# Kernel tuning notes

Measured on AMD Instinct MI355X. Metric: run time of the kernel, lower is better.

Reference implementation:

```python
import jax, jax.numpy as jnp
import numpy as np

EMBED_DIM = 1024
NUM_HEADS = 16
D_K = EMBED_DIM // NUM_HEADS


def setup_inputs() -> dict:
    key = jax.random.key(0)
    kx, kq, kk, kv, ko = jax.random.split(key, 5)
    scale = 1.0 / np.sqrt(EMBED_DIM)
    return {
        "x": jax.random.normal(kx, (4, 2048, EMBED_DIM), dtype=jnp.float32),
        # nn.Linear weights are [out, in]; we store them the same way.
        "w_q": jax.random.normal(kq, (EMBED_DIM, EMBED_DIM), dtype=jnp.float32) * scale,
        "w_k": jax.random.normal(kk, (EMBED_DIM, EMBED_DIM), dtype=jnp.float32) * scale,
        "w_v": jax.random.normal(kv, (EMBED_DIM, EMBED_DIM), dtype=jnp.float32) * scale,
        "w_o": jax.random.normal(ko, (EMBED_DIM, EMBED_DIM), dtype=jnp.float32) * scale,
    }


def reference(x, w_q, w_k, w_v, w_o):
    B, S, E = x.shape
    H, Dk = NUM_HEADS, D_K

    def proj(w):  # [B,S,E] @ [E,E]^T -> [B,H,S,Dk]
        y = jnp.einsum('bse,fe->bsf', x, w)
        return y.reshape(B, S, H, Dk).transpose(0, 2, 1, 3)

    q, k, v = proj(w_q), proj(w_k), proj(w_v)
    scores = jnp.einsum('bhsd,bhtd->bhst', q, k) / jnp.sqrt(jnp.float32(Dk))
    attn = jax.nn.softmax(scores, axis=-1)  # dropout p=0 -> identity
    out = jnp.einsum('bhst,bhtd->bhsd', attn, v)
    out = out.transpose(0, 2, 1, 3).reshape(B, S, E)
    return jnp.einsum('bse,fe->bsf', out, w_o)
```

## Files before the change

### kernel.cpp

```cpp
#include <hip/hip_runtime.h>
#include <stdint.h>

typedef unsigned short u16;
typedef __attribute__((ext_vector_type(8))) short bf16x8;
typedef __attribute__((ext_vector_type(4))) float f32x4;
typedef __attribute__((ext_vector_type(16))) float f32x16;

#define EMB 1024
#define SLEN 2048
#define NHD 16
#define DKH 64

__device__ __forceinline__ u16 f2bf(float f) {
  uint32_t u = __float_as_uint(f);
  u = (u + 0x7fffu + ((u >> 16) & 1u)) >> 16;
  return (u16)u;
}

__device__ __forceinline__ void load_lds16(const void* g, void* l) {
  __builtin_amdgcn_global_load_lds(
      (const __attribute__((address_space(1))) uint32_t*)g,
      (__attribute__((address_space(3))) uint32_t*)l, 16, 0, 0);
}

__global__ __launch_bounds__(256) void cvt_all(
    const float* __restrict__ x,
    const float* __restrict__ w0, const float* __restrict__ w1,
    const float* __restrict__ w2, const float* __restrict__ w3,
    u16* __restrict__ xo,
    u16* __restrict__ o0, u16* __restrict__ o1,
    u16* __restrict__ o2, u16* __restrict__ o3) {
  const int bid = blockIdx.x;
  const float* in;
  u16* out;
  int i;
  if (bid < 8192) {
    in = x; out = xo; i = bid * 256 + threadIdx.x;
  } else {
    const int ws = (bid - 8192) >> 10;
    in  = (ws == 0) ? w0 : (ws == 1) ? w1 : (ws == 2) ? w2 : w3;
    out = (ws == 0) ? o0 : (ws == 1) ? o1 : (ws == 2) ? o2 : o3;
    i = ((bid - 8192) & 1023) * 256 + threadIdx.x;
  }
  float4 v = ((const float4*)in)[i];
  union { u16 h[4]; uint64_t q; } o;
  o.h[0] = f2bf(v.x); o.h[1] = f2bf(v.y); o.h[2] = f2bf(v.z); o.h[3] = f2bf(v.w);
  ((uint64_t*)out)[i] = o.q;
}

template<int MODE>
__device__ __forceinline__ void gemm_body(const u16* __restrict__ A,
                                          const u16* __restrict__ W,
                                          void* __restrict__ C,
                                          int bm, int bn,
                                          u16* At, u16* Bt) {
  const int tid = threadIdx.x;
  const int l = tid & 63, w = tid >> 6;
  const int wm = w >> 2, wn = w & 3;
  const int lr = l & 15, lg = l >> 4;

  f32x4 acc[4][2] = {};

  const int sr = w * 16 + (l >> 2);
  const int sc = (l & 3) * 8;
  const u16* Ag = A + (size_t)(bm + sr) * EMB + sc;
  const u16* Wg = W + (size_t)(bn + sr) * EMB + sc;

  auto stage = [&](int buf, int k0) {
    load_lds16(Ag + k0, At + buf * 4096 + w * 512);
    load_lds16(Wg + k0, Bt + buf * 4096 + w * 512);
  };

  stage(0, 0);
  stage(1, 32);
  int cur = 0;

#pragma unroll 1
  for (int it = 0; it < 32; ++it) {
    if (it < 31)
      asm volatile("s_waitcnt vmcnt(2)" ::: "memory");
    else
      asm volatile("s_waitcnt vmcnt(0)" ::: "memory");
    __builtin_amdgcn_s_barrier();
    if (it < 30) {
      int nb = cur + 2; if (nb >= 3) nb -= 3;
      stage(nb, (it + 2) * 32);
    }
    bf16x8 af[4], bf[2];
#pragma unroll
    for (int i = 0; i < 4; ++i)
      af[i] = *(const bf16x8*)(At + cur * 4096 + (wm * 64 + i * 16 + lr) * 32 + lg * 8);
#pragma unroll
    for (int j = 0; j < 2; ++j)
      bf[j] = *(const bf16x8*)(Bt + cur * 4096 + (wn * 32 + j * 16 + lr) * 32 + lg * 8);
    __builtin_amdgcn_s_setprio(1);
#pragma unroll
    for (int i = 0; i < 4; ++i)
#pragma unroll
      for (int j = 0; j < 2; ++j)
        acc[i][j] = __builtin_amdgcn_mfma_f32_16x16x32_bf16(af[i], bf[j], acc[i][j], 0, 0, 0);
    __builtin_amdgcn_s_setprio(0);
    ++cur; if (cur == 3) cur = 0;
  }

  if (MODE == 2) {
#pragma unroll
    for (int i = 0; i < 4; ++i) {
      const int m0 = bm + wm * 64 + i * 16 + lg * 4;
      const int bb = m0 >> 11;
      const int ss = m0 & 2047;
#pragma unroll
      for (int j = 0; j < 2; ++j) {
        const int n = bn + wn * 32 + j * 16 + lr;
        const int hh = n >> 6, dd = n & 63;
        union { u16 h[4]; uint64_t q; } pk;
#pragma unroll
        for (int r = 0; r < 4; ++r) pk.h[r] = f2bf(acc[i][j][r]);
        *(uint64_t*)((u16*)C + ((size_t)((bb * 16 + hh) * 64 + dd)) * 2048 + ss) = pk.q;
      }
    }
  } else {
#pragma unroll
    for (int i = 0; i < 4; ++i) {
      const int mb = bm + wm * 64 + i * 16 + lg * 4;
#pragma unroll
      for (int j = 0; j < 2; ++j) {
        const int col = bn + wn * 32 + j * 16 + lr;
#pragma unroll
        for (int r = 0; r < 4; ++r) {
          float v = acc[i][j][r];
          if (MODE == 1) v *= 0.18033688011112042f;
          if (MODE == 3)
            ((float*)C)[(size_t)(mb + r) * EMB + col] = v;
          else
            ((u16*)C)[(size_t)(mb + r) * EMB + col] = f2bf(v);
        }
      }
    }
  }
}

__global__ __launch_bounds__(512) void gemm_qkv(
    const u16* __restrict__ A,
    const u16* __restrict__ wq, const u16* __restrict__ wk, const u16* __restrict__ wv,
    u16* __restrict__ Qo, u16* __restrict__ Ko, u16* __restrict__ Vo) {
  __shared__ __align__(16) u16 At[3 * 4096];
  __shared__ __align__(16) u16 Bt[3 * 4096];
  const int bid = blockIdx.x;
  const int wgid = (bid & 7) * 192 + (bid >> 3);
  const int z = wgid >> 9;
  const int rem = wgid & 511;
  const int bm = (rem >> 3) * 128, bn = (rem & 7) * 128;
  if (z == 0) gemm_body<1>(A, wq, Qo, bm, bn, At, Bt);
  else if (z == 1) gemm_body<0>(A, wk, Ko, bm, bn, At, Bt);
  else gemm_body<2>(A, wv, Vo, bm, bn, At, Bt);
}

__global__ __launch_bounds__(512) void gemm_out(const u16* __restrict__ A,
                                                const u16* __restrict__ W,
                                                float* __restrict__ C) {
  __shared__ __align__(16) u16 At[3 * 4096];
  __shared__ __align__(16) u16 Bt[3 * 4096];
  const int bid = blockIdx.x;
  const int wgid = (bid & 7) * 64 + (bid >> 3);
  const int bm = (wgid >> 3) * 128, bn = (wgid & 7) * 128;
  gemm_body<3>(A, W, C, bm, bn, At, Bt);
}

__global__ __launch_bounds__(512, 4) void attn_fwd(const u16* __restrict__ Q,
                                                   const u16* __restrict__ K,
                                                   const u16* __restrict__ VT,
                                                   u16* __restrict__ O) {
  __shared__ __align__(16) u16 lds[3][2][64 * 64];
  const int tid = threadIdx.x;
  const int l = tid & 63, w = tid >> 6;
  const int ql = l & 31, hi = l >> 5;
  const int bid = blockIdx.x;
  const int bh = (bid & 7) * 8 + (bid >> 6);
  const int qt = (bid >> 3) & 7;
  const int b = bh >> 4, h = bh & 15;
  const int qw = qt * 256 + w * 32;
  const size_t qkb = ((size_t)b * SLEN) * EMB + h * DKH;
  const size_t vb = (size_t)bh * DKH * SLEN;

  const int srow = tid >> 3;
  const int scb = ((tid & 7) * 16) ^ ((srow & 7) << 4);
  const u16* Ksrc = K + qkb + (size_t)srow * EMB + (scb >> 1);
  const u16* Vsrc = VT + vb + (size_t)srow * SLEN + (scb >> 1);

  auto stage = [&](int buf, int t) {
    load_lds16(Ksrc + (size_t)t * 64 * EMB, (char*)(&lds[buf][0][0]) + w * 1024);
    load_lds16(Vsrc + t * 64, (char*)(&lds[buf][1][0]) + w * 1024);
  };

  bf16x8 qf[4];
#pragma unroll
  for (int ks = 0; ks < 4; ++ks)
    qf[ks] = *(const bf16x8*)(Q + qkb + (size_t)(qw + ql) * EMB + ks * 16 + hi * 8);

  f32x16 accd[2] = {};
  float lsum = 0.f;

  stage(0, 0);
  stage(1, 1);
  int cur = 0;
#pragma unroll 1
  for (int t = 0; t < 32; ++t) {
    if (t < 30) {
      int nb = cur + 2; if (nb >= 3) nb -= 3;
      stage(nb, t + 2);
      asm volatile("s_waitcnt vmcnt(4)" ::: "memory");
    } else if (t == 30) {
      asm volatile("s_waitcnt vmcnt(2)" ::: "memory");
    } else {
      asm volatile("s_waitcnt vmcnt(0)" ::: "memory");
    }
    __builtin_amdgcn_s_barrier();

    const u16* Kt = &lds[cur][0][0];
    const u16* Vt = &lds[cur][1][0];

    f32x16 sacc[2] = {};
    __builtin_amdgcn_s_setprio(1);
#pragma unroll
    for (int kf2 = 0; kf2 < 2; ++kf2) {
      const int row = kf2 * 32 + ql;
      const int swz = (row & 7) << 4;
#pragma unroll
      for (int ks = 0; ks < 4; ++ks) {
        bf16x8 kf = *(const bf16x8*)((const char*)Kt + row * 128 +
                                     ((ks * 32 + hi * 16) ^ swz));
        sacc[kf2] = __builtin_amdgcn_mfma_f32_32x32x16_bf16(kf, qf[ks], sacc[kf2], 0, 0, 0);
      }
    }
    __builtin_amdgcn_s_setprio(0);

#pragma unroll
    for (int kf2 = 0; kf2 < 2; ++kf2)
#pragma unroll
      for (int r = 0; r < 16; ++r)
        sacc[kf2][r] = __builtin_amdgcn_exp2f(sacc[kf2][r]);
    float ps[8];
#pragma unroll
    for (int g = 0; g < 8; ++g) {
      const int kf2 = g >> 2, r0 = (g & 3) * 4;
      ps[g] = (sacc[kf2][r0] + sacc[kf2][r0 + 1]) + (sacc[kf2][r0 + 2] + sacc[kf2][r0 + 3]);
    }
    lsum += ((ps[0] + ps[1]) + (ps[2] + ps[3])) + ((ps[4] + ps[5]) + (ps[6] + ps[7]));

    __builtin_amdgcn_s_setprio(1);
#pragma unroll
    for (int ks = 0; ks < 4; ++ks) {
      const int kf2 = ks >> 1;
      const int e0 = (ks & 1) * 8;
      uint32_t a0, a1, b0, b1;
      asm("v_cvt_pk_bf16_f32 %0, %1, %2" : "=v"(a0) : "v"(sacc[kf2][e0 + 0]), "v"(sacc[kf2][e0 + 1]));
      asm("v_cvt_pk_bf16_f32 %0, %1, %2" : "=v"(a1) : "v"(sacc[kf2][e0 + 2]), "v"(sacc[kf2][e0 + 3]));
      asm("v_cvt_pk_bf16_f32 %0, %1, %2" : "=v"(b0) : "v"(sacc[kf2][e0 + 4]), "v"(sacc[kf2][e0 + 5]));
      asm("v_cvt_pk_bf16_f32 %0, %1, %2" : "=v"(b1) : "v"(sacc[kf2][e0 + 6]), "v"(sacc[kf2][e0 + 7]));
      asm("v_permlane32_swap_b32 %0, %1" : "+v"(a0), "+v"(b0));
      asm("v_permlane32_swap_b32 %0, %1" : "+v"(a1), "+v"(b1));
      union { uint32_t d[4]; bf16x8 v; } pa;
      pa.d[0] = a0; pa.d[1] = a1; pa.d[2] = b0; pa.d[3] = b1;
#pragma unroll
      for (int df = 0; df < 2; ++df) {
        const int vr = df * 32 + ql;
        bf16x8 vf = *(const bf16x8*)((const char*)Vt + vr * 128 +
                                     ((ks * 32 + hi * 16) ^ ((vr & 7) << 4)));
        accd[df] = __builtin_amdgcn_mfma_f32_32x32x16_bf16(pa.v, vf, accd[df], 0, 0, 0);
      }
    }
    __builtin_amdgcn_s_setprio(0);
    __builtin_amdgcn_s_barrier();
    ++cur; if (cur == 3) cur = 0;
  }

  lsum += __shfl_xor(lsum, 32, 64);

  __syncthreads();
  u16* slice = &lds[0][0][0] + w * 2048;
#pragma unroll
  for (int reg = 0; reg < 16; ++reg) {
    const int rowq = (reg & 3) + 8 * (reg >> 2) + 4 * hi;
    const float li = 1.0f / __shfl(lsum, rowq, 64);
    slice[rowq * 64 + ql] = f2bf(accd[0][reg] * li);
    slice[rowq * 64 + 32 + ql] = f2bf(accd[1][reg] * li);
  }
  asm volatile("s_waitcnt lgkmcnt(0)" ::: "memory");
#pragma unroll
  for (int j = 0; j < 4; ++j) {
    const int byteoff = j * 1024 + l * 16;
    const int row = byteoff >> 7;
    const int colB = byteoff & 127;
    bf16x8 vv = *(const bf16x8*)((const char*)slice + byteoff);
    *(bf16x8*)(O + qkb + (size_t)(qw + row) * EMB + (colB >> 1)) = vv;
  }
}

extern "C" void kernel_launch(void* const* d_in, const int* in_sizes, int n_in,
                              void* d_out, int out_size, void* d_ws, size_t ws_size,
                              hipStream_t stream) {
  const float* x  = (const float*)d_in[0];
  const float* wq = (const float*)d_in[1];
  const float* wk = (const float*)d_in[2];
  const float* wv = (const float*)d_in[3];
  const float* wo = (const float*)d_in[4];

  char* ws = (char*)d_ws;
  u16* xb  = (u16*)(ws + 0);
  u16* wqb = (u16*)(ws + 16777216);
  u16* wkb = (u16*)(ws + 18874368);
  u16* wvb = (u16*)(ws + 20971520);
  u16* wob = (u16*)(ws + 23068672);
  u16* Qb  = (u16*)(ws + 25165824);
  u16* Kb  = (u16*)(ws + 41943040);
  u16* VTb = (u16*)(ws + 58720256);
  u16* AO  = (u16*)(ws + 75497472);

  cvt_all<<<dim3(12288), 256, 0, stream>>>(x, wq, wk, wv, wo, xb, wqb, wkb, wvb, wob);

  gemm_qkv<<<dim3(1536), 512, 0, stream>>>(xb, wqb, wkb, wvb, Qb, Kb, VTb);
  attn_fwd<<<dim3(512), 512, 0, stream>>>(Qb, Kb, VTb, AO);
  gemm_out<<<dim3(512), 512, 0, stream>>>(AO, wob, (float*)d_out);
}
```

Baseline: 181.8 us.

## Switch GEMMs to 32x32x16 MFMA with 4 waves and 64x64 warp tiles

Rewrites the shared GEMM body to use 256-thread blocks (4 waves in a 2x2 grid), each wave computing a 64x64 subtile with 32x32x16 bf16 MFMAs instead of 16x16x32. Each thread now issues two async LDS loads per operand per stage, and the wait count is adjusted to match. Larger per-wave tiles raise register-level reuse and cut LDS reads per MFMA, but halving the waves per block reduces latency hiding. The epilogues are remapped to the 32x32 accumulator layout.

```diff
diff --git a/kernel.cpp b/kernel.cpp
--- a/kernel.cpp
+++ b/kernel.cpp
@@ -56,19 +56,25 @@
                                           u16* At, u16* Bt) {
   const int tid = threadIdx.x;
   const int l = tid & 63, w = tid >> 6;
-  const int wm = w >> 2, wn = w & 3;
-  const int lr = l & 15, lg = l >> 4;
-
-  f32x4 acc[4][2] = {};
-
-  const int sr = w * 16 + (l >> 2);
-  const int sc = (l & 3) * 8;
-  const u16* Ag = A + (size_t)(bm + sr) * EMB + sc;
-  const u16* Wg = W + (size_t)(bn + sr) * EMB + sc;
+  const int wm = w >> 1, wn = w & 1;
+  const int ql = l & 31, hi = l >> 5;
+
+  f32x16 acc[2][2] = {};
+
+  const int e0 = w * 1024 + l * 8;
+  const int r0 = e0 >> 5, c0 = e0 & 31;
+  const int e1 = e0 + 512;
+  const int r1 = e1 >> 5, c1 = e1 & 31;
+  const u16* Ag0 = A + (size_t)(bm + r0) * EMB + c0;
+  const u16* Ag1 = A + (size_t)(bm + r1) * EMB + c1;
+  const u16* Wg0 = W + (size_t)(bn + r0) * EMB + c0;
+  const u16* Wg1 = W + (size_t)(bn + r1) * EMB + c1;
 
   auto stage = [&](int buf, int k0) {
-    load_lds16(Ag + k0, At + buf * 4096 + w * 512);
-    load_lds16(Wg + k0, Bt + buf * 4096 + w * 512);
+    load_lds16(Ag0 + k0, At + buf * 4096 + w * 1024);
+    load_lds16(Ag1 + k0, At + buf * 4096 + w * 1024 + 512);
+    load_lds16(Wg0 + k0, Bt + buf * 4096 + w * 1024);
+    load_lds16(Wg1 + k0, Bt + buf * 4096 + w * 1024 + 512);
   };
 
   stage(0, 0);
@@ -78,7 +84,7 @@
 #pragma unroll 1
   for (int it = 0; it < 32; ++it) {
     if (it < 31)
-      asm volatile("s_waitcnt vmcnt(2)" ::: "memory");
+      asm volatile("s_waitcnt vmcnt(4)" ::: "memory");
     else
       asm volatile("s_waitcnt vmcnt(0)" ::: "memory");
     __builtin_amdgcn_s_barrier();
@@ -86,61 +92,66 @@
       int nb = cur + 2; if (nb >= 3) nb -= 3;
       stage(nb, (it + 2) * 32);
     }
-    bf16x8 af[4], bf[2];
-#pragma unroll
-    for (int i = 0; i < 4; ++i)
-      af[i] = *(const bf16x8*)(At + cur * 4096 + (wm * 64 + i * 16 + lr) * 32 + lg * 8);
-#pragma unroll
-    for (int j = 0; j < 2; ++j)
-      bf[j] = *(const bf16x8*)(Bt + cur * 4096 + (wn * 32 + j * 16 + lr) * 32 + lg * 8);
-    __builtin_amdgcn_s_setprio(1);
-#pragma unroll
-    for (int i = 0; i < 4; ++i)
-#pragma unroll
-      for (int j = 0; j < 2; ++j)
-        acc[i][j] = __builtin_amdgcn_mfma_f32_16x16x32_bf16(af[i], bf[j], acc[i][j], 0, 0, 0);
-    __builtin_amdgcn_s_setprio(0);
+    const u16* Ab = At + cur * 4096;
+    const u16* Bb = Bt + cur * 4096;
+#pragma unroll
+    for (int kk = 0; kk < 2; ++kk) {
+      bf16x8 af[2], bf[2];
+#pragma unroll
+      for (int f = 0; f < 2; ++f) {
+        af[f] = *(const bf16x8*)(Ab + (wm * 64 + f * 32 + ql) * 32 + kk * 16 + hi * 8);
+        bf[f] = *(const bf16x8*)(Bb + (wn * 64 + f * 32 + ql) * 32 + kk * 16 + hi * 8);
+      }
+      __builtin_amdgcn_s_setprio(1);
+#pragma unroll
+      for (int fi = 0; fi < 2; ++fi)
+#pragma unroll
+        for (int fj = 0; fj < 2; ++fj)
+          acc[fi][fj] = __builtin_amdgcn_mfma_f32_32x32x16_bf16(af[fi], bf[fj], acc[fi][fj], 0, 0, 0);
+      __builtin_amdgcn_s_setprio(0);
+    }
     ++cur; if (cur == 3) cur = 0;
   }
 
   if (MODE == 2) {
 #pragma unroll
-    for (int i = 0; i < 4; ++i) {
-      const int m0 = bm + wm * 64 + i * 16 + lg * 4;
-      const int bb = m0 >> 11;
-      const int ss = m0 & 2047;
-#pragma unroll
-      for (int j = 0; j < 2; ++j) {
-        const int n = bn + wn * 32 + j * 16 + lr;
-        const int hh = n >> 6, dd = n & 63;
-        union { u16 h[4]; uint64_t q; } pk;
-#pragma unroll
-        for (int r = 0; r < 4; ++r) pk.h[r] = f2bf(acc[i][j][r]);
-        *(uint64_t*)((u16*)C + ((size_t)((bb * 16 + hh) * 64 + dd)) * 2048 + ss) = pk.q;
-      }
-    }
+    for (int fi = 0; fi < 2; ++fi)
+#pragma unroll
+      for (int g = 0; g < 4; ++g) {
+        const int m0 = bm + wm * 64 + fi * 32 + g * 8 + hi * 4;
+        const int bb = m0 >> 11;
+        const int ss = m0 & 2047;
+#pragma unroll
+        for (int fj = 0; fj < 2; ++fj) {
+          const int n = bn + wn * 64 + fj * 32 + ql;
+          const int hh = n >> 6, dd = n & 63;
+          union { u16 h[4]; uint64_t q; } pk;
+#pragma unroll
+          for (int r = 0; r < 4; ++r) pk.h[r] = f2bf(acc[fi][fj][g * 4 + r]);
+          *(uint64_t*)((u16*)C + ((size_t)((bb * 16 + hh) * 64 + dd)) * 2048 + ss) = pk.q;
+        }
+      }
   } else {
 #pragma unroll
-    for (int i = 0; i < 4; ++i) {
-      const int mb = bm + wm * 64 + i * 16 + lg * 4;
-#pragma unroll
-      for (int j = 0; j < 2; ++j) {
-        const int col = bn + wn * 32 + j * 16 + lr;
-#pragma unroll
-        for (int r = 0; r < 4; ++r) {
-          float v = acc[i][j][r];
+    for (int fi = 0; fi < 2; ++fi)
+#pragma unroll
+      for (int fj = 0; fj < 2; ++fj) {
+        const int col = bn + wn * 64 + fj * 32 + ql;
+#pragma unroll
+        for (int reg = 0; reg < 16; ++reg) {
+          const int row = bm + wm * 64 + fi * 32 + (reg & 3) + 8 * (reg >> 2) + 4 * hi;
+          float v = acc[fi][fj][reg];
           if (MODE == 1) v *= 0.18033688011112042f;
           if (MODE == 3)
-            ((float*)C)[(size_t)(mb + r) * EMB + col] = v;
+            ((float*)C)[(size_t)row * EMB + col] = v;
           else
-            ((u16*)C)[(size_t)(mb + r) * EMB + col] = f2bf(v);
+            ((u16*)C)[(size_t)row * EMB + col] = f2bf(v);
         }
       }
-    }
-  }
-}
-
-__global__ __launch_bounds__(512) void gemm_qkv(
+  }
+}
+
+__global__ __launch_bounds__(256) void gemm_qkv(
     const u16* __restrict__ A,
     const u16* __restrict__ wq, const u16* __restrict__ wk, const u16* __restrict__ wv,
     u16* __restrict__ Qo, u16* __restrict__ Ko, u16* __restrict__ Vo) {
@@ -156,7 +167,7 @@
   else gemm_body<2>(A, wv, Vo, bm, bn, At, Bt);
 }
 
-__global__ __launch_bounds__(512) void gemm_out(const u16* __restrict__ A,
+__global__ __launch_bounds__(256) void gemm_out(const u16* __restrict__ A,
                                                 const u16* __restrict__ W,
                                                 float* __restrict__ C) {
   __shared__ __align__(16) u16 At[3 * 4096];
@@ -319,7 +330,7 @@
 
   cvt_all<<<dim3(12288), 256, 0, stream>>>(x, wq, wk, wv, wo, xb, wqb, wkb, wvb, wob);
 
-  gemm_qkv<<<dim3(1536), 512, 0, stream>>>(xb, wqb, wkb, wvb, Qb, Kb, VTb);
+  gemm_qkv<<<dim3(1536), 256, 0, stream>>>(xb, wqb, wkb, wvb, Qb, Kb, VTb);
   attn_fwd<<<dim3(512), 512, 0, stream>>>(Qb, Kb, VTb, AO);
-  gemm_out<<<dim3(512), 512, 0, stream>>>(AO, wob, (float*)d_out);
-}
+  gemm_out<<<dim3(512), 256, 0, stream>>>(AO, wob, (float*)d_out);
+}
```

After: 191.7 us. 5.4% more time.
